# Kernel optimization log

Hardware: AMD Instinct MI355X
Metric: run time of the kernel (lower is better)

The kernel has to match this reference:

```python
import jax, jax.numpy as jnp
import numpy as np

HEADS = 8
DIM_HEAD = 64


def setup_inputs() -> dict:
    key = jax.random.key(0)
    ks = jax.random.split(key, 8)
    B, L, m = 4, 1024, 64
    Dq, Dc = 512, 256
    inner = HEADS * DIM_HEAD  # 512
    x = jax.random.normal(ks[0], (B, L, Dq), dtype=jnp.float32)
    context = jax.random.normal(ks[1], (B, L, m, Dc), dtype=jnp.float32)
    mask = jax.random.randint(ks[2], (B, L, m), 0, 2).astype(bool)
    # guarantee at least one valid token per (b,l) row
    mask = mask.at[:, :, 0].set(True)
    bias = jax.random.normal(ks[3], (B, L, m), dtype=jnp.float32)
    s = 0.02
    Wq = jax.random.normal(ks[4], (Dq, inner), dtype=jnp.float32) * s
    Wk = jax.random.normal(ks[5], (Dc, inner), dtype=jnp.float32) * s
    Wv = jax.random.normal(ks[6], (Dc, inner), dtype=jnp.float32) * s
    Wo = jax.random.normal(ks[7], (inner, Dq), dtype=jnp.float32) * s
    bo = jnp.zeros((Dq,), dtype=jnp.float32)
    return {"x": x, "context": context, "mask": mask, "bias": bias,
            "Wq": Wq, "Wk": Wk, "Wv": Wv, "Wo": Wo, "bo": bo}


def reference(x, context, mask, bias, Wq, Wk, Wv, Wo, bo):
    B, L, Dq = x.shape
    m = context.shape[2]
    scale = DIM_HEAD ** (-0.5)
    # projections
    Q = (x @ Wq).reshape(B, L, HEADS, DIM_HEAD)                 # b l h d
    K = (context @ Wk).reshape(B, L, m, HEADS, DIM_HEAD)        # b l m h d
    V = (context @ Wv).reshape(B, L, m, HEADS, DIM_HEAD)        # b l m h d
    scores = jnp.einsum('blhd,blmhd->blhm', Q, K) * scale       # b l h m
    scores = scores + bias[:, :, None, :]
    scores = jnp.where(mask[:, :, None, :], scores, -jnp.inf)
    attn = jax.nn.softmax(scores, axis=-1)
    out = jnp.einsum('blhm,blmhd->blhd', attn, V).reshape(B, L, HEADS * DIM_HEAD)
    return out @ Wo + bo
```

## Files before the change

### kernel.cpp

```cpp
#include <hip/hip_runtime.h>
#include <cstddef>


typedef __attribute__((ext_vector_type(8))) short short8;
typedef __attribute__((ext_vector_type(4))) float float4v;

__device__ __forceinline__ short f2bf(float f) {
  unsigned u = __float_as_uint(f);
  return (short)((u + 0x7fffu + ((u >> 16) & 1u)) >> 16);
}

__global__ __launch_bounds__(256) void k_cvt(const float* __restrict__ x,
                                             const float* __restrict__ Wk,
                                             const float* __restrict__ Wv,
                                             short* __restrict__ xb,
                                             short* __restrict__ Wkb,
                                             short* __restrict__ Wvb) {
  size_t i4 = ((size_t)blockIdx.x * 256 + threadIdx.x) * 4;
  const float* src; short* dst; size_t off;
  if (i4 < 2097152)       { src = x;  dst = xb;  off = i4; }
  else if (i4 < 2228224)  { src = Wk; dst = Wkb; off = i4 - 2097152; }
  else                    { src = Wv; dst = Wvb; off = i4 - 2228224; }
  float4 v = *(const float4*)(src + off);
  short4 o; o.x = f2bf(v.x); o.y = f2bf(v.y); o.z = f2bf(v.z); o.w = f2bf(v.w);
  *(short4*)(dst + off) = o;
}

__global__ __launch_bounds__(256) void k_tcvt(const float* __restrict__ in,
                                              short* __restrict__ out) {
  int id = blockIdx.x * 256 + threadIdx.x;
  int k = id >> 9, n = id & 511;
  out[(size_t)n * 512 + k] = f2bf(in[(size_t)k * 512 + n]);
}

__global__ __launch_bounds__(256) void k_mm(const short* __restrict__ A,
                                            const short* __restrict__ Bt,
                                            const float* __restrict__ bias,
                                            void* __restrict__ C,
                                            int lda, int ldb, int ldc, int K,
                                            int bShift, int bMask, int bHS, int crossAK,
                                            float scale, int storeBF16) {
  __shared__ short As[128 * 72];
  __shared__ short Bs[128 * 72];
  int t = threadIdx.x;
  int n0 = blockIdx.x * 128, m0 = blockIdx.y * 128;
  int hb = n0 >> bShift;
  const short* aBase = A + (size_t)m0 * lda + (size_t)hb * crossAK;
  const short* bBase = Bt + (size_t)(n0 & bMask) * ldb + (size_t)hb * bHS;
  int w = t >> 6, l = t & 63;
  int wm = w & 1, wn = w >> 1;
  int li = l & 15, kq = l >> 4;
  float4v acc[4][4];
#pragma unroll
  for (int i = 0; i < 4; ++i)
#pragma unroll
    for (int j = 0; j < 4; ++j) acc[i][j] = (float4v){0.f, 0.f, 0.f, 0.f};

  for (int k0 = 0; k0 < K; k0 += 64) {
    __syncthreads();
#pragma unroll
    for (int p = 0; p < 4; ++p) {
      int i = p * 256 + t, row = i >> 3, kq8 = i & 7;
      *(uint4*)&As[row * 72 + kq8 * 8] = *(const uint4*)(aBase + (size_t)row * lda + k0 + kq8 * 8);
      *(uint4*)&Bs[row * 72 + kq8 * 8] = *(const uint4*)(bBase + (size_t)row * ldb + k0 + kq8 * 8);
    }
    __syncthreads();
#pragma unroll
    for (int kk = 0; kk < 2; ++kk) {
      short8 af[4], bfr[4];
#pragma unroll
      for (int i = 0; i < 4; ++i) {
        af[i]  = *(const short8*)&As[(wm * 64 + i * 16 + li) * 72 + kk * 32 + kq * 8];
        bfr[i] = *(const short8*)&Bs[(wn * 64 + i * 16 + li) * 72 + kk * 32 + kq * 8];
      }
#pragma unroll
      for (int mi = 0; mi < 4; ++mi)
#pragma unroll
        for (int ni = 0; ni < 4; ++ni)
          acc[mi][ni] = __builtin_amdgcn_mfma_f32_16x16x32_bf16(af[mi], bfr[ni], acc[mi][ni], 0, 0, 0);
    }
  }
#pragma unroll
  for (int ni = 0; ni < 4; ++ni) {
    int col = n0 + wn * 64 + ni * 16 + li;
    float bv = bias ? bias[col] : 0.f;
#pragma unroll
    for (int mi = 0; mi < 4; ++mi)
#pragma unroll
      for (int r = 0; r < 4; ++r) {
        int row = m0 + wm * 64 + mi * 16 + kq * 4 + r;
        float v = fmaf(acc[mi][ni][r], scale, bv);
        if (storeBF16) ((short*)C)[(size_t)row * ldc + col] = f2bf(v);
        else           ((float*)C)[(size_t)row * ldc + col] = v;
      }
  }
}

__global__ __launch_bounds__(256) void k_attn(const float* __restrict__ ctx,
                                              const float* __restrict__ Qk,
                                              const float* __restrict__ bias,
                                              const int* __restrict__ mask,
                                              short* __restrict__ CA) {
  __shared__ float ctxs[64 * 132];
  __shared__ float qks[2048];
  __shared__ float sc[512];
  __shared__ float bs[64];
  __shared__ int   ms[64];
  int t = threadIdx.x;
  int r = blockIdx.x;
  const float* ctxr = ctx + (size_t)r * 16384;

  const float4* q4 = (const float4*)(Qk + (size_t)r * 2048);
  ((float4*)qks)[t]       = q4[t];
  ((float4*)qks)[t + 256] = q4[t + 256];
  if (t < 64) { bs[t] = bias[(size_t)r * 64 + t]; ms[t] = mask[(size_t)r * 64 + t]; }

  int m_ = t & 63, h0 = t >> 6;
  float s0 = 0.f, s1 = 0.f;
  for (int kk = 0; kk < 2; ++kk) {
    __syncthreads();
#pragma unroll
    for (int i = 0; i < 8; ++i) {
      int l = t + i * 256;
      int m = l >> 5, c4 = l & 31;
      float4 v = *(const float4*)(ctxr + m * 256 + kk * 128 + c4 * 4);
      *(float4*)(ctxs + m * 132 + c4 * 4) = v;
    }
    __syncthreads();
    const float* cp = ctxs + m_ * 132;
    const float* q0 = qks + h0 * 256 + kk * 128;
    const float* q1 = q0 + 1024;
#pragma unroll 8
    for (int c4 = 0; c4 < 32; ++c4) {
      float4 cv = *(const float4*)(cp + c4 * 4);
      float4 qa = *(const float4*)(q0 + c4 * 4);
      float4 qb = *(const float4*)(q1 + c4 * 4);
      s0 = fmaf(cv.x, qa.x, s0); s0 = fmaf(cv.y, qa.y, s0);
      s0 = fmaf(cv.z, qa.z, s0); s0 = fmaf(cv.w, qa.w, s0);
      s1 = fmaf(cv.x, qb.x, s1); s1 = fmaf(cv.y, qb.y, s1);
      s1 = fmaf(cv.z, qb.z, s1); s1 = fmaf(cv.w, qb.w, s1);
    }
  }
  bool valid = ms[m_] != 0;
  float b = bs[m_];
  s0 = valid ? s0 + b : -INFINITY;
  s1 = valid ? s1 + b : -INFINITY;
  float mx0 = s0, mx1 = s1;
#pragma unroll
  for (int o = 32; o > 0; o >>= 1) {
    mx0 = fmaxf(mx0, __shfl_xor(mx0, o, 64));
    mx1 = fmaxf(mx1, __shfl_xor(mx1, o, 64));
  }
  float e0 = __expf(s0 - mx0), e1 = __expf(s1 - mx1);
  float sm0 = e0, sm1 = e1;
#pragma unroll
  for (int o = 32; o > 0; o >>= 1) {
    sm0 += __shfl_xor(sm0, o, 64);
    sm1 += __shfl_xor(sm1, o, 64);
  }
  sc[m_ * 8 + h0]     = e0 / sm0;
  sc[m_ * 8 + h0 + 4] = e1 / sm1;
  __syncthreads();
  float acc[8] = {};
#pragma unroll 4
  for (int m = 0; m < 64; ++m) {
    float cv = ctxr[m * 256 + t];
    float4 w0 = *(const float4*)&sc[m * 8];
    float4 w1 = *(const float4*)&sc[m * 8 + 4];
    acc[0] = fmaf(w0.x, cv, acc[0]); acc[1] = fmaf(w0.y, cv, acc[1]);
    acc[2] = fmaf(w0.z, cv, acc[2]); acc[3] = fmaf(w0.w, cv, acc[3]);
    acc[4] = fmaf(w1.x, cv, acc[4]); acc[5] = fmaf(w1.y, cv, acc[5]);
    acc[6] = fmaf(w1.z, cv, acc[6]); acc[7] = fmaf(w1.w, cv, acc[7]);
  }
  short* car = CA + (size_t)r * 2048;
#pragma unroll
  for (int hh = 0; hh < 8; ++hh) car[hh * 256 + t] = f2bf(acc[hh]);
}

extern "C" void kernel_launch(void* const* d_in, const int* in_sizes, int n_in,
                              void* d_out, int out_size, void* d_ws, size_t ws_size,
                              hipStream_t stream) {
  const float* x    = (const float*)d_in[0];
  const float* ctx  = (const float*)d_in[1];
  const int*   mask = (const int*)d_in[2];
  const float* bias = (const float*)d_in[3];
  const float* Wq   = (const float*)d_in[4];
  const float* Wk   = (const float*)d_in[5];
  const float* Wv   = (const float*)d_in[6];
  const float* Wo   = (const float*)d_in[7];
  const float* bo   = (const float*)d_in[8];
  float* out = (float*)d_out;

  char* ws = (char*)d_ws;
  short* xb    = (short*)(ws);
  short* Qb    = (short*)(ws + (4u << 20));
  float* Qk    = (float*)(ws + (8u << 20));
  short* CAb   = (short*)(ws + (40u << 20));
  short* WqTb  = (short*)(ws + (56u << 20));
  short* WoTb  = (short*)(ws + (56u << 20) + (512u << 10));
  short* Wkb   = (short*)(ws + (57u << 20));
  short* Wvb   = (short*)(ws + (57u << 20) + (256u << 10));
  short* WvoTb = (short*)(ws + (58u << 20));

  hipLaunchKernelGGL(k_cvt,  dim3(2304), dim3(256), 0, stream, x, Wk, Wv, xb, Wkb, Wvb);
  hipLaunchKernelGGL(k_tcvt, dim3(1024), dim3(256), 0, stream, Wq, WqTb);
  hipLaunchKernelGGL(k_tcvt, dim3(1024), dim3(256), 0, stream, Wo, WoTb);
  hipLaunchKernelGGL(k_mm, dim3(16, 4), dim3(256), 0, stream,
                     WoTb, Wvb, (const float*)nullptr, WvoTb,
                     512, 512, 2048, 64, 8, 255, 64, 64, 1.0f, 1);
  hipLaunchKernelGGL(k_mm, dim3(4, 32), dim3(256), 0, stream,
                     xb, WqTb, (const float*)nullptr, Qb,
                     512, 512, 512, 512, 31, 0x7fffffff, 0, 0, 1.0f, 1);
  hipLaunchKernelGGL(k_mm, dim3(16, 32), dim3(256), 0, stream,
                     Qb, Wkb, (const float*)nullptr, Qk,
                     512, 512, 2048, 64, 8, 255, 64, 64, 0.125f, 0);
  hipLaunchKernelGGL(k_attn, dim3(4096), dim3(256), 0, stream, ctx, Qk, bias, mask, CAb);
  hipLaunchKernelGGL(k_mm, dim3(4, 32), dim3(256), 0, stream,
                     CAb, WvoTb, bo, out,
                     2048, 2048, 512, 2048, 31, 0x7fffffff, 0, 0, 1.0f, 0);
}
```

Baseline: 485.2 us.

## Use bf16 MFMA for attention scores and context aggregation in k_attn

Rewrites the attention kernel so both the score computation (context·Qk) and the weighted context sum run on bf16 MFMA instructions instead of scalar fp32 FMAs. Context rows are converted to bf16 once, staged in shared memory, and transposed through register shuffles for the second matmul. Qk is now stored as bf16, which halves its traffic, and launch bounds request three blocks per CU. The cost is reduced precision in scores and weights, plus extra shuffle and shared-memory transposition work.

```diff
diff --git a/kernel.cpp b/kernel.cpp
--- a/kernel.cpp
+++ b/kernel.cpp
@@ -96,55 +96,66 @@
   }
 }
 
-__global__ __launch_bounds__(256) void k_attn(const float* __restrict__ ctx,
-                                              const float* __restrict__ Qk,
-                                              const float* __restrict__ bias,
-                                              const int* __restrict__ mask,
-                                              short* __restrict__ CA) {
-  __shared__ float ctxs[64 * 132];
-  __shared__ float qks[2048];
-  __shared__ float sc[512];
+__global__ __launch_bounds__(256, 3) void k_attn(const float* __restrict__ ctx,
+                                                 const short* __restrict__ Qkb,
+                                                 const float* __restrict__ bias,
+                                                 const int* __restrict__ mask,
+                                                 short* __restrict__ CA) {
+  __shared__ __align__(16) short uni[256 * 72];
+  __shared__ __align__(16) float S[64][17];
+  __shared__ __align__(16) short attn_b[16][72];
   __shared__ float bs[64];
-  __shared__ int   ms[64];
+  __shared__ int   msk[64];
+
   int t = threadIdx.x;
   int r = blockIdx.x;
+  int l = t & 63, w = t >> 6;
+  int li = l & 15, kq = l >> 4;
+
   const float* ctxr = ctx + (size_t)r * 16384;
-
-  const float4* q4 = (const float4*)(Qk + (size_t)r * 2048);
-  ((float4*)qks)[t]       = q4[t];
-  ((float4*)qks)[t + 256] = q4[t + 256];
-  if (t < 64) { bs[t] = bias[(size_t)r * 64 + t]; ms[t] = mask[(size_t)r * 64 + t]; }
+  const short* qrow = Qkb + (size_t)r * 2048;
+
+  uint* az = (uint*)&attn_b[8][0];
+  az[t] = 0;
+  if (t < 32) az[256 + t] = 0;
+
+  int hq = l & 7;
+  short8 qf[8];
+#pragma unroll
+  for (int ks = 0; ks < 8; ++ks)
+    qf[ks] = *(const short8*)(qrow + hq * 256 + ks * 32 + kq * 8);
+
+  if (t < 64) { bs[t] = bias[(size_t)r * 64 + t]; msk[t] = mask[(size_t)r * 64 + t]; }
+
+  short (*mc)[264] = (short (*)[264])uni;
+  short (*cm)[72]  = (short (*)[72])uni;
+
+  short4 sv[16];
+#pragma unroll
+  for (int i = 0; i < 16; ++i) {
+    int m = w * 16 + i;
+    float4 v = *(const float4*)(ctxr + m * 256 + l * 4);
+    short4 b4; b4.x = f2bf(v.x); b4.y = f2bf(v.y); b4.z = f2bf(v.z); b4.w = f2bf(v.w);
+    sv[i] = b4;
+    *(short4*)&mc[m][l * 4] = b4;
+  }
+  __syncthreads();
+
+  float4v sacc = (float4v){0.f, 0.f, 0.f, 0.f};
+#pragma unroll
+  for (int ks = 0; ks < 8; ++ks) {
+    short8 af = *(const short8*)&mc[w * 16 + li][ks * 32 + kq * 8];
+    sacc = __builtin_amdgcn_mfma_f32_16x16x32_bf16(af, qf[ks], sacc, 0, 0, 0);
+  }
+#pragma unroll
+  for (int rg = 0; rg < 4; ++rg) S[w * 16 + kq * 4 + rg][li] = sacc[rg];
+  __syncthreads();
 
   int m_ = t & 63, h0 = t >> 6;
-  float s0 = 0.f, s1 = 0.f;
-  for (int kk = 0; kk < 2; ++kk) {
-    __syncthreads();
-#pragma unroll
-    for (int i = 0; i < 8; ++i) {
-      int l = t + i * 256;
-      int m = l >> 5, c4 = l & 31;
-      float4 v = *(const float4*)(ctxr + m * 256 + kk * 128 + c4 * 4);
-      *(float4*)(ctxs + m * 132 + c4 * 4) = v;
-    }
-    __syncthreads();
-    const float* cp = ctxs + m_ * 132;
-    const float* q0 = qks + h0 * 256 + kk * 128;
-    const float* q1 = q0 + 1024;
-#pragma unroll 8
-    for (int c4 = 0; c4 < 32; ++c4) {
-      float4 cv = *(const float4*)(cp + c4 * 4);
-      float4 qa = *(const float4*)(q0 + c4 * 4);
-      float4 qb = *(const float4*)(q1 + c4 * 4);
-      s0 = fmaf(cv.x, qa.x, s0); s0 = fmaf(cv.y, qa.y, s0);
-      s0 = fmaf(cv.z, qa.z, s0); s0 = fmaf(cv.w, qa.w, s0);
-      s1 = fmaf(cv.x, qb.x, s1); s1 = fmaf(cv.y, qb.y, s1);
-      s1 = fmaf(cv.z, qb.z, s1); s1 = fmaf(cv.w, qb.w, s1);
-    }
-  }
-  bool valid = ms[m_] != 0;
+  bool valid = msk[m_] != 0;
   float b = bs[m_];
-  s0 = valid ? s0 + b : -INFINITY;
-  s1 = valid ? s1 + b : -INFINITY;
+  float s0 = valid ? S[m_][h0] + b : -INFINITY;
+  float s1 = valid ? S[m_][h0 + 4] + b : -INFINITY;
   float mx0 = s0, mx1 = s1;
 #pragma unroll
   for (int o = 32; o > 0; o >>= 1) {
@@ -158,23 +169,55 @@
     sm0 += __shfl_xor(sm0, o, 64);
     sm1 += __shfl_xor(sm1, o, 64);
   }
-  sc[m_ * 8 + h0]     = e0 / sm0;
-  sc[m_ * 8 + h0 + 4] = e1 / sm1;
+  attn_b[h0][m_]     = f2bf(e0 / sm0);
+  attn_b[h0 + 4][m_] = f2bf(e1 / sm1);
+
+#pragma unroll
+  for (int p = 0; p < 4; ++p) {
+    int c  = l + p * 64;
+    int sl = (l >> 2) + p * 16;
+#pragma unroll
+    for (int k = 0; k < 4; ++k) {
+      int wd[4];
+#pragma unroll
+      for (int j = 0; j < 4; ++j) {
+        int2 two = *(int2*)&sv[4 * k + j];
+        int wx = __shfl(two.x, sl, 64);
+        int wy = __shfl(two.y, sl, 64);
+        wd[j] = (l & 2) ? wy : wx;
+      }
+      short4 o;
+      o.x = (l & 1) ? (short)(wd[0] >> 16) : (short)wd[0];
+      o.y = (l & 1) ? (short)(wd[1] >> 16) : (short)wd[1];
+      o.z = (l & 1) ? (short)(wd[2] >> 16) : (short)wd[2];
+      o.w = (l & 1) ? (short)(wd[3] >> 16) : (short)wd[3];
+      *(short4*)&cm[c][w * 16 + k * 4] = o;
+    }
+  }
   __syncthreads();
-  float acc[8] = {};
-#pragma unroll 4
-  for (int m = 0; m < 64; ++m) {
-    float cv = ctxr[m * 256 + t];
-    float4 w0 = *(const float4*)&sc[m * 8];
-    float4 w1 = *(const float4*)&sc[m * 8 + 4];
-    acc[0] = fmaf(w0.x, cv, acc[0]); acc[1] = fmaf(w0.y, cv, acc[1]);
-    acc[2] = fmaf(w0.z, cv, acc[2]); acc[3] = fmaf(w0.w, cv, acc[3]);
-    acc[4] = fmaf(w1.x, cv, acc[4]); acc[5] = fmaf(w1.y, cv, acc[5]);
-    acc[6] = fmaf(w1.z, cv, acc[6]); acc[7] = fmaf(w1.w, cv, acc[7]);
-  }
+
+  short8 bfr[2];
+#pragma unroll
+  for (int ks = 0; ks < 2; ++ks)
+    bfr[ks] = *(const short8*)&attn_b[li][ks * 32 + kq * 8];
+  float4v ca[4];
+#pragma unroll
+  for (int mi = 0; mi < 4; ++mi) ca[mi] = (float4v){0.f, 0.f, 0.f, 0.f};
+#pragma unroll
+  for (int mi = 0; mi < 4; ++mi)
+#pragma unroll
+    for (int ks = 0; ks < 2; ++ks) {
+      short8 af = *(const short8*)&cm[w * 64 + mi * 16 + li][ks * 32 + kq * 8];
+      ca[mi] = __builtin_amdgcn_mfma_f32_16x16x32_bf16(af, bfr[ks], ca[mi], 0, 0, 0);
+    }
   short* car = CA + (size_t)r * 2048;
-#pragma unroll
-  for (int hh = 0; hh < 8; ++hh) car[hh * 256 + t] = f2bf(acc[hh]);
+  if (li < 8) {
+#pragma unroll
+    for (int mi = 0; mi < 4; ++mi)
+#pragma unroll
+      for (int rg = 0; rg < 4; ++rg)
+        car[li * 256 + w * 64 + mi * 16 + kq * 4 + rg] = f2bf(ca[mi][rg]);
+  }
 }
 
 extern "C" void kernel_launch(void* const* d_in, const int* in_sizes, int n_in,
@@ -194,13 +237,13 @@
   char* ws = (char*)d_ws;
   short* xb    = (short*)(ws);
   short* Qb    = (short*)(ws + (4u << 20));
-  float* Qk    = (float*)(ws + (8u << 20));
-  short* CAb   = (short*)(ws + (40u << 20));
-  short* WqTb  = (short*)(ws + (56u << 20));
-  short* WoTb  = (short*)(ws + (56u << 20) + (512u << 10));
-  short* Wkb   = (short*)(ws + (57u << 20));
-  short* Wvb   = (short*)(ws + (57u << 20) + (256u << 10));
-  short* WvoTb = (short*)(ws + (58u << 20));
+  short* Qkb   = (short*)(ws + (8u << 20));
+  short* CAb   = (short*)(ws + (24u << 20));
+  short* WqTb  = (short*)(ws + (40u << 20));
+  short* WoTb  = (short*)(ws + (40u << 20) + (512u << 10));
+  short* Wkb   = (short*)(ws + (41u << 20));
+  short* Wvb   = (short*)(ws + (41u << 20) + (256u << 10));
+  short* WvoTb = (short*)(ws + (42u << 20));
 
   hipLaunchKernelGGL(k_cvt,  dim3(2304), dim3(256), 0, stream, x, Wk, Wv, xb, Wkb, Wvb);
   hipLaunchKernelGGL(k_tcvt, dim3(1024), dim3(256), 0, stream, Wq, WqTb);
@@ -212,9 +255,9 @@
                      xb, WqTb, (const float*)nullptr, Qb,
                      512, 512, 512, 512, 31, 0x7fffffff, 0, 0, 1.0f, 1);
   hipLaunchKernelGGL(k_mm, dim3(16, 32), dim3(256), 0, stream,
-                     Qb, Wkb, (const float*)nullptr, Qk,
-                     512, 512, 2048, 64, 8, 255, 64, 64, 0.125f, 0);
-  hipLaunchKernelGGL(k_attn, dim3(4096), dim3(256), 0, stream, ctx, Qk, bias, mask, CAb);
+                     Qb, Wkb, (const float*)nullptr, Qkb,
+                     512, 512, 2048, 64, 8, 255, 64, 64, 0.125f, 1);
+  hipLaunchKernelGGL(k_attn, dim3(4096), dim3(256), 0, stream, ctx, Qkb, bias, mask, CAb);
   hipLaunchKernelGGL(k_mm, dim3(4, 32), dim3(256), 0, stream,
                      CAb, WvoTb, bo, out,
                      2048, 2048, 512, 2048, 31, 0x7fffffff, 0, 0, 1.0f, 0);
```

Result: faster. 465.0 us (-4.1%).
